# Kernel tuning notes

Measured on AMD Instinct MI355X. Metric: run time of the kernel, lower is better.

## Reference

```python
import jax, jax.numpy as jnp
import numpy as np


def setup_inputs() -> dict:
    key = jax.random.key(0)
    B, L, S, H, E, D = 2, 2048, 2048, 16, 64, 64
    k1, k2, k3, k4 = jax.random.split(key, 4)
    return {
        "queries": jax.random.normal(k1, (B, L, H, E), dtype=jnp.float32),
        "keys": jax.random.normal(k2, (B, S, H, E), dtype=jnp.float32),
        "values": jax.random.normal(k3, (B, S, H, D), dtype=jnp.float32),
        # stands in for torch.randn(B, H, L, S) inside the original forward
        "scores": jax.random.normal(k4, (B, H, L, S), dtype=jnp.float32),
    }


def reference(queries, keys, values, scores):
    # Faithful to ZZYAttention.forward with mask_flag=True, attn_mask=None,
    # dropout p=0 (eval), output_attention=False. queries/keys are unused by
    # the original math (scores are the random presoftmax tensor).
    B, L, H, E = queries.shape
    S = values.shape[1]
    # first softmax over the raw (random) scores
    w = jax.nn.softmax(scores, axis=-1)                      # [B,H,L,S]
    # TriangularCausalMask: True strictly above the diagonal -> masked_fill(-inf)
    causal = jnp.triu(jnp.ones((L, S), dtype=bool), k=1)     # [L,S]
    w = jnp.where(causal[None, None, :, :], -jnp.inf, w)
    # second softmax after masking (masked entries become exactly 0)
    A = jax.nn.softmax(w, axis=-1)                           # [B,H,L,S]
    # attention-value contraction
    V = jnp.einsum('bhls,bshd->blhd', A, values)             # [B,L,H,D]
    return V
```

## Files before the change

### kernel.cpp

```cpp
#include <hip/hip_runtime.h>

constexpr int Bc = 2, Hc = 16, Lc = 2048, Sc = 2048, Dc = 64;
constexpr int TL = 16;
constexpr int TJ = 128;
constexpr int NT = 256;
constexpr int PP = 136;
constexpr int PV = 136;

typedef __attribute__((ext_vector_type(8))) short short8;
typedef __attribute__((ext_vector_type(4))) float f32x4;

__device__ __forceinline__ unsigned short f2bf(float x) {
  unsigned u = __float_as_uint(x);
  u += 0x7FFF + ((u >> 16) & 1);
  return (unsigned short)(u >> 16);
}
__device__ __forceinline__ float wave_max(float v) {
#pragma unroll
  for (int m = 32; m >= 1; m >>= 1) v = fmaxf(v, __shfl_xor(v, m));
  return v;
}
__device__ __forceinline__ float wave_sum(float v) {
#pragma unroll
  for (int m = 32; m >= 1; m >>= 1) v += __shfl_xor(v, m);
  return v;
}
__device__ __forceinline__ float half_sum(float v) {
#pragma unroll
  for (int m = 16; m >= 1; m >>= 1) v += __shfl_xor(v, m);
  return v;
}

__global__ __launch_bounds__(256) void transpose_v(const float* __restrict__ V,
                                                   unsigned short* __restrict__ Vt) {
  const int st = blockIdx.x, h = blockIdx.y, b = blockIdx.z;
  const int s0 = st * 64, tid = threadIdx.x;
  __shared__ float t[64][65];
  const float* vb = V + ((size_t)(b * Sc + s0) * Hc + h) * Dc;
#pragma unroll
  for (int e = 0; e < 4; ++e) {
    int f = tid + 256 * e, si = f >> 4, dq = f & 15;
    float4 v = *(const float4*)(vb + (size_t)si * Hc * Dc + dq * 4);
    t[si][dq * 4 + 0] = v.x; t[si][dq * 4 + 1] = v.y;
    t[si][dq * 4 + 2] = v.z; t[si][dq * 4 + 3] = v.w;
  }
  __syncthreads();
  const int d = tid >> 2, sq = tid & 3;
  unsigned pk[8];
#pragma unroll
  for (int k = 0; k < 8; ++k) {
    int s = sq * 16 + 2 * k;
    pk[k] = (unsigned)f2bf(t[s][d]) | ((unsigned)f2bf(t[s + 1][d]) << 16);
  }
  unsigned short* dst = Vt + ((size_t)((b * Hc + h) * Dc + d)) * Sc + s0 + sq * 16;
  uint4* dv = (uint4*)dst;
  dv[0] = make_uint4(pk[0], pk[1], pk[2], pk[3]);
  dv[1] = make_uint4(pk[4], pk[5], pk[6], pk[7]);
}

__global__ __launch_bounds__(NT) void zzy_attn(
    const unsigned short* __restrict__ Vt,
    const float* __restrict__ scores,
    float* __restrict__ out) {
  const int lt = blockIdx.x, h = blockIdx.y, b = blockIdx.z;
  const int l0 = lt * TL, tid = threadIdx.x;
  const int lane = tid & 63, wv = tid >> 6;

  __shared__ __align__(16) unsigned short vT[64 * PV];
  __shared__ __align__(16) unsigned short pt[TL * PP];
  __shared__ float s_m1[TL], s_iz1[TL], z2acc[TL];

  const size_t score_bh = (size_t)(b * Hc + h) * Lc * Sc;

#pragma unroll
  for (int t = 0; t < 4; ++t) {
    const int r = wv * 4 + t;
    const float4* row = (const float4*)(scores + score_bh + (size_t)(l0 + r) * Sc);
    float4 v[8];
#pragma unroll
    for (int e = 0; e < 8; ++e) v[e] = row[lane + 64 * e];
    float m = -1e30f;
#pragma unroll
    for (int e = 0; e < 8; ++e)
      m = fmaxf(m, fmaxf(fmaxf(v[e].x, v[e].y), fmaxf(v[e].z, v[e].w)));
    m = wave_max(m);
    float s = 0.f;
#pragma unroll
    for (int e = 0; e < 8; ++e)
      s += __expf(v[e].x - m) + __expf(v[e].y - m) +
           __expf(v[e].z - m) + __expf(v[e].w - m);
    s = wave_sum(s);
    if (lane == 0) { s_m1[r] = m; s_iz1[r] = 1.0f / s; }
  }
  __syncthreads();

  const int m16 = lane & 15, q = lane >> 4;
  f32x4 acc = {0.f, 0.f, 0.f, 0.f};
  float z0 = 0.f, z1 = 0.f;
  const int r0 = tid >> 5;
  const unsigned short* vtb = Vt + (size_t)((b * Hc + h) * Dc) * Sc;
  const int ntiles = (l0 + TL - 1) / TJ + 1;

  for (int jt = 0; jt < ntiles; ++jt) {
    const int j0 = jt * TJ;
#pragma unroll
    for (int e = 0; e < 4; ++e) {
      int f = tid + 256 * e, ch = f & 15, d = f >> 4;
      uint4 v = *(const uint4*)(vtb + (size_t)d * Sc + j0 + ch * 8);
      *(uint4*)&vT[d * PV + ch * 8] = v;
    }
#pragma unroll
    for (int e = 0; e < 2; ++e) {
      int f = tid + 256 * e, r = f >> 5, jc = f & 31;
      int l = l0 + r;
      float4 s = *(const float4*)(scores + score_bh + (size_t)l * Sc + j0 + jc * 4);
      float m1 = s_m1[r], iz = s_iz1[r];
      int jb = j0 + jc * 4;
      float p0 = (jb + 0 <= l) ? __expf(__expf(s.x - m1) * iz) : 0.f;
      float p1 = (jb + 1 <= l) ? __expf(__expf(s.y - m1) * iz) : 0.f;
      float p2 = (jb + 2 <= l) ? __expf(__expf(s.z - m1) * iz) : 0.f;
      float p3 = (jb + 3 <= l) ? __expf(__expf(s.w - m1) * iz) : 0.f;
      if (e == 0) z0 += p0 + p1 + p2 + p3; else z1 += p0 + p1 + p2 + p3;
      uint2 pk;
      pk.x = (unsigned)f2bf(p0) | ((unsigned)f2bf(p1) << 16);
      pk.y = (unsigned)f2bf(p2) | ((unsigned)f2bf(p3) << 16);
      *(uint2*)&pt[r * PP + jc * 4] = pk;
    }
    __syncthreads();
#pragma unroll
    for (int ks = 0; ks < 4; ++ks) {
      short8 af = *(const short8*)&pt[m16 * PP + ks * 32 + q * 8];
      short8 bf = *(const short8*)&vT[(16 * wv + m16) * PV + ks * 32 + q * 8];
      acc = __builtin_amdgcn_mfma_f32_16x16x32_bf16(af, bf, acc, 0, 0, 0);
    }
    __syncthreads();
  }

  float zz0 = half_sum(z0), zz1 = half_sum(z1);
  if ((tid & 31) == 0) { z2acc[r0] = zz0; z2acc[r0 + 8] = zz1; }
  __syncthreads();

#pragma unroll
  for (int reg = 0; reg < 4; ++reg) {
    int row = q * 4 + reg;
    float o = acc[reg] / z2acc[row];
    out[((size_t)(b * Lc + l0 + row) * Hc + h) * Dc + 16 * wv + m16] = o;
  }
}

extern "C" void kernel_launch(void* const* d_in, const int* in_sizes, int n_in,
                              void* d_out, int out_size, void* d_ws,
                              size_t ws_size, hipStream_t stream) {
  const float* values = (const float*)d_in[2];
  const float* scores = (const float*)d_in[3];
  float* out = (float*)d_out;
  unsigned short* Vt = (unsigned short*)d_ws;

  transpose_v<<<dim3(Sc / 64, Hc, Bc), 256, 0, stream>>>(values, Vt);
  zzy_attn<<<dim3(Lc / TL, Hc, Bc), NT, 0, stream>>>(Vt, scores, out);
}
```

Measured before the change: 751.8 us.

## Double-buffer P tile, prefetch scores, and read V fragments directly from global

Replaces the LDS staging of the transposed V tile with direct per-lane global loads of the MFMA B fragments. It also double-buffers the probability tile so one barrier per iteration is enough, and prefetches the next score tile into registers before the barrier. The aim is to cut LDS traffic and barrier count and to overlap score loads with compute. In exchange the V fragment loads are smaller and less coalesced, and they now sit directly in front of the MFMAs.

```diff
diff --git a/kernel.cpp b/kernel.cpp
--- a/kernel.cpp
+++ b/kernel.cpp
@@ -5,7 +5,6 @@
 constexpr int TJ = 128;
 constexpr int NT = 256;
 constexpr int PP = 136;
-constexpr int PV = 136;
 
 typedef __attribute__((ext_vector_type(8))) short short8;
 typedef __attribute__((ext_vector_type(4))) float f32x4;
@@ -66,8 +65,7 @@
   const int l0 = lt * TL, tid = threadIdx.x;
   const int lane = tid & 63, wv = tid >> 6;
 
-  __shared__ __align__(16) unsigned short vT[64 * PV];
-  __shared__ __align__(16) unsigned short pt[TL * PP];
+  __shared__ __align__(16) unsigned short pt[2][TL * PP];
   __shared__ float s_m1[TL], s_iz1[TL], z2acc[TL];
 
   const size_t score_bh = (size_t)(b * Hc + h) * Lc * Sc;
@@ -98,42 +96,62 @@
   f32x4 acc = {0.f, 0.f, 0.f, 0.f};
   float z0 = 0.f, z1 = 0.f;
   const int r0 = tid >> 5;
-  const unsigned short* vtb = Vt + (size_t)((b * Hc + h) * Dc) * Sc;
+
+  const int pjc = tid & 31;
+  const int jq = pjc * 4;
+  const float* srowA = scores + score_bh + (size_t)(l0 + r0) * Sc + jq;
+  const float* srowB = srowA + (size_t)8 * Sc;
+  const float m1a = s_m1[r0],     iza = s_iz1[r0];
+  const float m1b = s_m1[r0 + 8], izb = s_iz1[r0 + 8];
+  const int la = l0 + r0, lb = la + 8;
+
+  const unsigned short* vrow =
+      Vt + ((size_t)((b * Hc + h) * Dc + 16 * wv + m16)) * Sc + q * 8;
+
   const int ntiles = (l0 + TL - 1) / TJ + 1;
+
+  float4 sA = *(const float4*)(srowA);
+  float4 sB = *(const float4*)(srowB);
 
   for (int jt = 0; jt < ntiles; ++jt) {
     const int j0 = jt * TJ;
-#pragma unroll
-    for (int e = 0; e < 4; ++e) {
-      int f = tid + 256 * e, ch = f & 15, d = f >> 4;
-      uint4 v = *(const uint4*)(vtb + (size_t)d * Sc + j0 + ch * 8);
-      *(uint4*)&vT[d * PV + ch * 8] = v;
-    }
-#pragma unroll
-    for (int e = 0; e < 2; ++e) {
-      int f = tid + 256 * e, r = f >> 5, jc = f & 31;
-      int l = l0 + r;
-      float4 s = *(const float4*)(scores + score_bh + (size_t)l * Sc + j0 + jc * 4);
-      float m1 = s_m1[r], iz = s_iz1[r];
-      int jb = j0 + jc * 4;
-      float p0 = (jb + 0 <= l) ? __expf(__expf(s.x - m1) * iz) : 0.f;
-      float p1 = (jb + 1 <= l) ? __expf(__expf(s.y - m1) * iz) : 0.f;
-      float p2 = (jb + 2 <= l) ? __expf(__expf(s.z - m1) * iz) : 0.f;
-      float p3 = (jb + 3 <= l) ? __expf(__expf(s.w - m1) * iz) : 0.f;
-      if (e == 0) z0 += p0 + p1 + p2 + p3; else z1 += p0 + p1 + p2 + p3;
+    unsigned short* pb = pt[jt & 1];
+
+    {
+      const int jb = j0 + jq;
+      float p0 = (jb + 0 <= la) ? __expf(__expf(sA.x - m1a) * iza) : 0.f;
+      float p1 = (jb + 1 <= la) ? __expf(__expf(sA.y - m1a) * iza) : 0.f;
+      float p2 = (jb + 2 <= la) ? __expf(__expf(sA.z - m1a) * iza) : 0.f;
+      float p3 = (jb + 3 <= la) ? __expf(__expf(sA.w - m1a) * iza) : 0.f;
+      z0 += p0 + p1 + p2 + p3;
       uint2 pk;
       pk.x = (unsigned)f2bf(p0) | ((unsigned)f2bf(p1) << 16);
       pk.y = (unsigned)f2bf(p2) | ((unsigned)f2bf(p3) << 16);
-      *(uint2*)&pt[r * PP + jc * 4] = pk;
+      *(uint2*)&pb[r0 * PP + jq] = pk;
+
+      float q0 = (jb + 0 <= lb) ? __expf(__expf(sB.x - m1b) * izb) : 0.f;
+      float q1 = (jb + 1 <= lb) ? __expf(__expf(sB.y - m1b) * izb) : 0.f;
+      float q2 = (jb + 2 <= lb) ? __expf(__expf(sB.z - m1b) * izb) : 0.f;
+      float q3 = (jb + 3 <= lb) ? __expf(__expf(sB.w - m1b) * izb) : 0.f;
+      z1 += q0 + q1 + q2 + q3;
+      pk.x = (unsigned)f2bf(q0) | ((unsigned)f2bf(q1) << 16);
+      pk.y = (unsigned)f2bf(q2) | ((unsigned)f2bf(q3) << 16);
+      *(uint2*)&pb[(r0 + 8) * PP + jq] = pk;
     }
+
+    if (jt + 1 < ntiles) {
+      sA = *(const float4*)(srowA + j0 + TJ);
+      sB = *(const float4*)(srowB + j0 + TJ);
+    }
+
     __syncthreads();
+
 #pragma unroll
     for (int ks = 0; ks < 4; ++ks) {
-      short8 af = *(const short8*)&pt[m16 * PP + ks * 32 + q * 8];
-      short8 bf = *(const short8*)&vT[(16 * wv + m16) * PV + ks * 32 + q * 8];
+      short8 af = *(const short8*)&pb[m16 * PP + ks * 32 + q * 8];
+      short8 bf = *(const short8*)(vrow + j0 + ks * 32);
       acc = __builtin_amdgcn_mfma_f32_16x16x32_bf16(af, bf, acc, 0, 0, 0);
     }
-    __syncthreads();
   }
 
   float zz0 = half_sum(z0), zz1 = half_sum(z1);
```

Measured after the change: 755.1 us. About the same (+0.4%).
